# Optimization experiments

Hardware: AMD Instinct MI355X
Metric: run time of the kernel (lower is better)

Reference implementation:

```python
import jax, jax.numpy as jnp
from jax import lax
import numpy as np

WIN = 15
PAD = WIN // 2  # floor(15/2) = 7


def _box_sum(x):
    """Sum over a 15x15 window, stride 1, zero padding 7 (same as F.conv2d
    with an all-ones [1,1,15,15] filter). Done separably (H then W) for
    efficiency; math is identical to the dense ones-filter conv."""
    kh = jnp.ones((1, 1, WIN, 1), x.dtype)
    kw = jnp.ones((1, 1, 1, WIN), x.dtype)
    x = lax.conv_general_dilated(x, kh, (1, 1), [(PAD, PAD), (0, 0)])
    x = lax.conv_general_dilated(x, kw, (1, 1), [(0, 0), (PAD, PAD)])
    return x


def setup_inputs() -> dict:
    key = jax.random.key(0)
    k1, k2 = jax.random.split(key)
    B, C, H, W = 16, 1, 512, 512
    I = jax.random.uniform(k1, (B, C, H, W), dtype=jnp.float32)
    J = jax.random.uniform(k2, (B, C, H, W), dtype=jnp.float32)
    return {"I": I, "J": J}


def reference(I, J):
    win_size = jnp.asarray(WIN * WIN, I.dtype)

    I_sum = _box_sum(I)
    J_sum = _box_sum(J)
    I2_sum = _box_sum(I * I)
    J2_sum = _box_sum(J * J)
    IJ_sum = _box_sum(I * J)

    u_I = I_sum / win_size
    u_J = J_sum / win_size

    cross = IJ_sum - u_J * I_sum - u_I * J_sum + u_I * u_J * win_size
    I_var = I2_sum - 2 * u_I * I_sum + u_I * u_I * win_size
    J_var = J2_sum - 2 * u_J * J_sum + u_J * u_J * win_size

    # NOTE: faithful to the torch code — cc is a GLOBAL scalar ratio,
    # so torch.mean(cc) == cc.
    cc = jnp.sum(cross) / jnp.sqrt(jnp.sum(I_var) * jnp.sum(J_var))
    return -cc
```

## Files before the change

### kernel.cpp

```cpp
#include <hip/hip_runtime.h>
#include <math.h>


#define IMG_H 512
#define IMG_W 512
#define NB    16
#define TW    64
#define TH    32
#define HALO  7
#define SPAN_R 46
#define SPAN_C 78
#define LSTR  78
#define VSTR  79
#define NTX   8
#define NTY   16
#define NBLK  (NB * NTX * NTY)

__device__ __forceinline__ float winw(int i) {
    int a = i < 7 ? i : 7;
    int b = (511 - i) < 7 ? (511 - i) : 7;
    return (float)(a + b + 1);
}

__global__ __launch_bounds__(256) void ncc_main(const float* __restrict__ I,
                                                const float* __restrict__ J,
                                                float* __restrict__ partials) {
    __shared__ float lI[SPAN_R * LSTR];
    __shared__ float lJ[SPAN_R * LSTR];
    __shared__ float vI[TH * VSTR];
    __shared__ float vJ[TH * VSTR];
    __shared__ float red[4 * 6];

    const int tid = threadIdx.x;
    const int tx = blockIdx.x, ty = blockIdx.y, bz = blockIdx.z;
    const int R0 = ty * TH - HALO;
    const int C0 = tx * TW - HALO;
    const float* Ib = I + (size_t)bz * IMG_H * IMG_W;
    const float* Jb = J + (size_t)bz * IMG_H * IMG_W;

    float a0 = 0.f, a1 = 0.f, a2 = 0.f;

    for (int k = tid; k < SPAN_R * SPAN_C; k += 256) {
        int r = k / SPAN_C;
        int c = k - r * SPAN_C;
        int gr = R0 + r, gc = C0 + c;
        float iv = 0.0f, jv = 0.0f;
        if ((unsigned)gr < (unsigned)IMG_H && (unsigned)gc < (unsigned)IMG_W) {
            int gidx = gr * IMG_W + gc;
            iv = Ib[gidx];
            jv = Jb[gidx];
        }
        lI[r * LSTR + c] = iv;
        lJ[r * LSTR + c] = jv;
        if (r >= HALO && r < HALO + TH && c >= HALO && c < HALO + TW) {
            float w = winw(gr) * winw(gc);
            a0 += iv * jv * w;
            a1 += iv * iv * w;
            a2 += jv * jv * w;
        }
    }
    __syncthreads();

    {
        int cid = tid % SPAN_C;
        int chunk = tid / SPAN_C;
        if (chunk < 3) {
            int r0 = chunk * 11;
            int nr = (chunk == 2) ? 10 : 11;
            float sI = 0.0f, sJ = 0.0f;
            #pragma unroll
            for (int dr = 0; dr < 15; ++dr) {
                sI += lI[(r0 + dr) * LSTR + cid];
                sJ += lJ[(r0 + dr) * LSTR + cid];
            }
            vI[r0 * VSTR + cid] = sI;
            vJ[r0 * VSTR + cid] = sJ;
            for (int r = r0 + 1; r < r0 + nr; ++r) {
                sI += lI[(r + 14) * LSTR + cid] - lI[(r - 1) * LSTR + cid];
                sJ += lJ[(r + 14) * LSTR + cid] - lJ[(r - 1) * LSTR + cid];
                vI[r * VSTR + cid] = sI;
                vJ[r * VSTR + cid] = sJ;
            }
        }
    }
    __syncthreads();

    float a3 = 0.f, a4 = 0.f, a5 = 0.f;
    {
        int r = tid & 31;
        int ch = tid >> 5;
        int c0 = ch * 8;
        int base = r * VSTR + c0;
        float va[22], vb[22];
        #pragma unroll
        for (int i = 0; i < 22; ++i) {
            va[i] = vI[base + i];
            vb[i] = vJ[base + i];
        }
        float sI = 0.0f, sJ = 0.0f;
        #pragma unroll
        for (int i = 0; i < 15; ++i) { sI += va[i]; sJ += vb[i]; }
        a3 += sI * sJ;
        a4 += sI * sI;
        a5 += sJ * sJ;
        #pragma unroll
        for (int i = 1; i < 8; ++i) {
            sI += va[i + 14] - va[i - 1];
            sJ += vb[i + 14] - vb[i - 1];
            a3 += sI * sJ;
            a4 += sI * sI;
            a5 += sJ * sJ;
        }
    }

    float vals[6] = {a0, a1, a2, a3, a4, a5};
    #pragma unroll
    for (int k = 0; k < 6; ++k) {
        float v = vals[k];
        #pragma unroll
        for (int off = 32; off > 0; off >>= 1) v += __shfl_down(v, off, 64);
        vals[k] = v;
    }
    int wave = tid >> 6, lane = tid & 63;
    if (lane == 0) {
        #pragma unroll
        for (int k = 0; k < 6; ++k) red[wave * 6 + k] = vals[k];
    }
    __syncthreads();
    if (tid == 0) {
        int bidx = (bz * NTY + ty) * NTX + tx;
        #pragma unroll
        for (int k = 0; k < 6; ++k) {
            partials[bidx * 6 + k] = red[k] + red[6 + k] + red[12 + k] + red[18 + k];
        }
    }
}

__global__ __launch_bounds__(256) void ncc_finalize(const float* __restrict__ partials,
                                                    float* __restrict__ out) {
    __shared__ double red[4 * 6];
    int tid = threadIdx.x;
    double acc[6] = {0, 0, 0, 0, 0, 0};
    for (int b = tid; b < NBLK; b += 256) {
        #pragma unroll
        for (int k = 0; k < 6; ++k) acc[k] += (double)partials[b * 6 + k];
    }
    #pragma unroll
    for (int k = 0; k < 6; ++k) {
        double v = acc[k];
        #pragma unroll
        for (int off = 32; off > 0; off >>= 1) v += __shfl_down(v, off, 64);
        acc[k] = v;
    }
    int wave = tid >> 6, lane = tid & 63;
    if (lane == 0) {
        #pragma unroll
        for (int k = 0; k < 6; ++k) red[wave * 6 + k] = acc[k];
    }
    __syncthreads();
    if (tid == 0) {
        double s[6];
        #pragma unroll
        for (int k = 0; k < 6; ++k) s[k] = red[k] + red[6 + k] + red[12 + k] + red[18 + k];
        double A = s[0], Bv = s[1], Cv = s[2], D = s[3], E = s[4], F = s[5];
        double num = A - D / 225.0;
        double varI = Bv - E / 225.0;
        double varJ = Cv - F / 225.0;
        double cc = num / sqrt(varI * varJ);
        out[0] = (float)(-cc);
    }
}

extern "C" void kernel_launch(void* const* d_in, const int* in_sizes, int n_in,
                              void* d_out, int out_size, void* d_ws, size_t ws_size,
                              hipStream_t stream) {
    const float* I = (const float*)d_in[0];
    const float* J = (const float*)d_in[1];
    float* partials = (float*)d_ws;

    dim3 grid(NTX, NTY, NB);
    ncc_main<<<grid, 256, 0, stream>>>(I, J, partials);
    ncc_finalize<<<1, 256, 0, stream>>>(partials, (float*)d_out);
}
```

Baseline: 99.64 us.

## Compute horizontal box sums in registers via float4 loads and fuse finalize via atomic counter

Each thread now loads a 32-wide row segment of I and J with float4 reads into registers and computes the horizontal 15-wide running sums directly. It writes interleaved float2 partial sums to shared memory, replacing the old full-tile staging and the vertical-first shared-memory pass. The separate finalize kernel is removed: the last block, found with an atomic counter and thread fences, does the double-precision global reduction. This cuts shared-memory traffic and one kernel launch, but adds a memset, atomic serialization, and heavy register use (64 floats per thread) that may lower occupancy.

```diff
diff --git a/kernel.cpp b/kernel.cpp
--- a/kernel.cpp
+++ b/kernel.cpp
@@ -7,11 +7,8 @@
 #define NB    16
 #define TW    64
 #define TH    32
-#define HALO  7
 #define SPAN_R 46
-#define SPAN_C 78
-#define LSTR  78
-#define VSTR  79
+#define STR2  65
 #define NTX   8
 #define NTY   16
 #define NBLK  (NB * NTX * NTY)
@@ -24,92 +21,87 @@
 
 __global__ __launch_bounds__(256) void ncc_main(const float* __restrict__ I,
                                                 const float* __restrict__ J,
-                                                float* __restrict__ partials) {
-    __shared__ float lI[SPAN_R * LSTR];
-    __shared__ float lJ[SPAN_R * LSTR];
-    __shared__ float vI[TH * VSTR];
-    __shared__ float vJ[TH * VSTR];
-    __shared__ float red[4 * 6];
+                                                float* __restrict__ partials,
+                                                unsigned* __restrict__ counter,
+                                                float* __restrict__ out) {
+    __shared__ float2 H[SPAN_R * STR2];
+    __shared__ float redf[4 * 6];
+    __shared__ double redd[4 * 6];
+    __shared__ int lastflag;
 
     const int tid = threadIdx.x;
     const int tx = blockIdx.x, ty = blockIdx.y, bz = blockIdx.z;
-    const int R0 = ty * TH - HALO;
-    const int C0 = tx * TW - HALO;
+    const int R0 = ty * TH - 7;
+    const int C0 = tx * TW;
     const float* Ib = I + (size_t)bz * IMG_H * IMG_W;
     const float* Jb = J + (size_t)bz * IMG_H * IMG_W;
 
     float a0 = 0.f, a1 = 0.f, a2 = 0.f;
 
-    for (int k = tid; k < SPAN_R * SPAN_C; k += 256) {
-        int r = k / SPAN_C;
-        int c = k - r * SPAN_C;
-        int gr = R0 + r, gc = C0 + c;
-        float iv = 0.0f, jv = 0.0f;
-        if ((unsigned)gr < (unsigned)IMG_H && (unsigned)gc < (unsigned)IMG_W) {
-            int gidx = gr * IMG_W + gc;
-            iv = Ib[gidx];
-            jv = Jb[gidx];
+    if (tid < SPAN_R * 4) {
+        int r = tid >> 2;
+        int run = tid & 3;
+        int gr = R0 + r;
+        int c0 = C0 + run * 16;
+        int gb = c0 - 8;
+        bool rowok = ((unsigned)gr < (unsigned)IMG_H);
+        float rI[32], rJ[32];
+        #pragma unroll
+        for (int q = 0; q < 8; ++q) {
+            int gc = gb + q * 4;
+            float4 iv = make_float4(0.f, 0.f, 0.f, 0.f);
+            float4 jv = make_float4(0.f, 0.f, 0.f, 0.f);
+            if (rowok && (unsigned)gc < (unsigned)IMG_W) {
+                iv = *reinterpret_cast<const float4*>(Ib + gr * IMG_W + gc);
+                jv = *reinterpret_cast<const float4*>(Jb + gr * IMG_W + gc);
+            }
+            rI[4 * q + 0] = iv.x; rI[4 * q + 1] = iv.y;
+            rI[4 * q + 2] = iv.z; rI[4 * q + 3] = iv.w;
+            rJ[4 * q + 0] = jv.x; rJ[4 * q + 1] = jv.y;
+            rJ[4 * q + 2] = jv.z; rJ[4 * q + 3] = jv.w;
         }
-        lI[r * LSTR + c] = iv;
-        lJ[r * LSTR + c] = jv;
-        if (r >= HALO && r < HALO + TH && c >= HALO && c < HALO + TW) {
-            float w = winw(gr) * winw(gc);
-            a0 += iv * jv * w;
-            a1 += iv * iv * w;
-            a2 += jv * jv * w;
+        if (r >= 7 && r < 7 + TH) {
+            float wr = winw(gr);
+            #pragma unroll
+            for (int t = 0; t < 16; ++t) {
+                float w = wr * winw(c0 + t);
+                float iv = rI[t + 8], jv = rJ[t + 8];
+                a0 += iv * jv * w;
+                a1 += iv * iv * w;
+                a2 += jv * jv * w;
+            }
         }
-    }
-    __syncthreads();
-
-    {
-        int cid = tid % SPAN_C;
-        int chunk = tid / SPAN_C;
-        if (chunk < 3) {
-            int r0 = chunk * 11;
-            int nr = (chunk == 2) ? 10 : 11;
-            float sI = 0.0f, sJ = 0.0f;
-            #pragma unroll
-            for (int dr = 0; dr < 15; ++dr) {
-                sI += lI[(r0 + dr) * LSTR + cid];
-                sJ += lJ[(r0 + dr) * LSTR + cid];
-            }
-            vI[r0 * VSTR + cid] = sI;
-            vJ[r0 * VSTR + cid] = sJ;
-            for (int r = r0 + 1; r < r0 + nr; ++r) {
-                sI += lI[(r + 14) * LSTR + cid] - lI[(r - 1) * LSTR + cid];
-                sJ += lJ[(r + 14) * LSTR + cid] - lJ[(r - 1) * LSTR + cid];
-                vI[r * VSTR + cid] = sI;
-                vJ[r * VSTR + cid] = sJ;
-            }
+        float hI = 0.f, hJ = 0.f;
+        #pragma unroll
+        for (int d = 1; d <= 15; ++d) { hI += rI[d]; hJ += rJ[d]; }
+        float2* Hrow = &H[r * STR2 + run * 16];
+        Hrow[0] = make_float2(hI, hJ);
+        #pragma unroll
+        for (int t = 1; t < 16; ++t) {
+            hI += rI[t + 15] - rI[t];
+            hJ += rJ[t + 15] - rJ[t];
+            Hrow[t] = make_float2(hI, hJ);
         }
     }
     __syncthreads();
 
     float a3 = 0.f, a4 = 0.f, a5 = 0.f;
     {
-        int r = tid & 31;
-        int ch = tid >> 5;
-        int c0 = ch * 8;
-        int base = r * VSTR + c0;
-        float va[22], vb[22];
+        int c = tid & 63;
+        int band = tid >> 6;
+        int rb = band * 8;
+        float2 win[22];
         #pragma unroll
-        for (int i = 0; i < 22; ++i) {
-            va[i] = vI[base + i];
-            vb[i] = vJ[base + i];
-        }
-        float sI = 0.0f, sJ = 0.0f;
+        for (int i = 0; i < 22; ++i) win[i] = H[(rb + i) * STR2 + c];
+        float sI = 0.f, sJ = 0.f;
         #pragma unroll
-        for (int i = 0; i < 15; ++i) { sI += va[i]; sJ += vb[i]; }
-        a3 += sI * sJ;
-        a4 += sI * sI;
-        a5 += sJ * sJ;
+        for (int i = 0; i < 15; ++i) { sI += win[i].x; sJ += win[i].y; }
+        a3 += sI * sJ; a4 += sI * sI; a5 += sJ * sJ;
         #pragma unroll
         for (int i = 1; i < 8; ++i) {
-            sI += va[i + 14] - va[i - 1];
-            sJ += vb[i + 14] - vb[i - 1];
-            a3 += sI * sJ;
-            a4 += sI * sI;
-            a5 += sJ * sJ;
+            sI += win[i + 14].x - win[i - 1].x;
+            sJ += win[i + 14].y - win[i - 1].y;
+            a3 += sI * sJ; a4 += sI * sI; a5 += sJ * sJ;
         }
     }
 
@@ -124,50 +116,52 @@
     int wave = tid >> 6, lane = tid & 63;
     if (lane == 0) {
         #pragma unroll
-        for (int k = 0; k < 6; ++k) red[wave * 6 + k] = vals[k];
+        for (int k = 0; k < 6; ++k) redf[wave * 6 + k] = vals[k];
     }
     __syncthreads();
     if (tid == 0) {
         int bidx = (bz * NTY + ty) * NTX + tx;
         #pragma unroll
         for (int k = 0; k < 6; ++k) {
-            partials[bidx * 6 + k] = red[k] + red[6 + k] + red[12 + k] + red[18 + k];
+            partials[bidx * 6 + k] = redf[k] + redf[6 + k] + redf[12 + k] + redf[18 + k];
         }
-    }
-}
-
-__global__ __launch_bounds__(256) void ncc_finalize(const float* __restrict__ partials,
-                                                    float* __restrict__ out) {
-    __shared__ double red[4 * 6];
-    int tid = threadIdx.x;
-    double acc[6] = {0, 0, 0, 0, 0, 0};
-    for (int b = tid; b < NBLK; b += 256) {
-        #pragma unroll
-        for (int k = 0; k < 6; ++k) acc[k] += (double)partials[b * 6 + k];
-    }
-    #pragma unroll
-    for (int k = 0; k < 6; ++k) {
-        double v = acc[k];
-        #pragma unroll
-        for (int off = 32; off > 0; off >>= 1) v += __shfl_down(v, off, 64);
-        acc[k] = v;
-    }
-    int wave = tid >> 6, lane = tid & 63;
-    if (lane == 0) {
-        #pragma unroll
-        for (int k = 0; k < 6; ++k) red[wave * 6 + k] = acc[k];
+        __threadfence();
+        unsigned old = atomicAdd(counter, 1u);
+        lastflag = (old == (unsigned)(NBLK - 1)) ? 1 : 0;
     }
     __syncthreads();
-    if (tid == 0) {
-        double s[6];
+
+    if (lastflag) {
+        __threadfence();
+        double acc[6] = {0, 0, 0, 0, 0, 0};
+        for (int b = tid; b < NBLK; b += 256) {
+            #pragma unroll
+            for (int k = 0; k < 6; ++k) acc[k] += (double)partials[b * 6 + k];
+        }
         #pragma unroll
-        for (int k = 0; k < 6; ++k) s[k] = red[k] + red[6 + k] + red[12 + k] + red[18 + k];
-        double A = s[0], Bv = s[1], Cv = s[2], D = s[3], E = s[4], F = s[5];
-        double num = A - D / 225.0;
-        double varI = Bv - E / 225.0;
-        double varJ = Cv - F / 225.0;
-        double cc = num / sqrt(varI * varJ);
-        out[0] = (float)(-cc);
+        for (int k = 0; k < 6; ++k) {
+            double v = acc[k];
+            #pragma unroll
+            for (int off = 32; off > 0; off >>= 1) v += __shfl_down(v, off, 64);
+            acc[k] = v;
+        }
+        if (lane == 0) {
+            #pragma unroll
+            for (int k = 0; k < 6; ++k) redd[wave * 6 + k] = acc[k];
+        }
+        __syncthreads();
+        if (tid == 0) {
+            double s[6];
+            #pragma unroll
+            for (int k = 0; k < 6; ++k)
+                s[k] = redd[k] + redd[6 + k] + redd[12 + k] + redd[18 + k];
+            double A = s[0], Bv = s[1], Cv = s[2], D = s[3], E = s[4], F = s[5];
+            double num = A - D / 225.0;
+            double varI = Bv - E / 225.0;
+            double varJ = Cv - F / 225.0;
+            double cc = num / sqrt(varI * varJ);
+            out[0] = (float)(-cc);
+        }
     }
 }
 
@@ -177,8 +171,9 @@
     const float* I = (const float*)d_in[0];
     const float* J = (const float*)d_in[1];
     float* partials = (float*)d_ws;
+    unsigned* counter = (unsigned*)((char*)d_ws + NBLK * 6 * sizeof(float));
 
+    hipMemsetAsync(counter, 0, sizeof(unsigned), stream);
     dim3 grid(NTX, NTY, NB);
-    ncc_main<<<grid, 256, 0, stream>>>(I, J, partials);
-    ncc_finalize<<<1, 256, 0, stream>>>(partials, (float*)d_out);
+    ncc_main<<<grid, 256, 0, stream>>>(I, J, partials, counter, (float*)d_out);
 }
```

Result: slower. 136.0 us (+36.5%).

## Split box-filter NCC into separate vertical and horizontal pass kernels

Applied to the files above, without the earlier changes.

Replaces the single fused tiled kernel, which loads a haloed 2D tile into LDS, with two kernels. A vertical running-sum kernel streams columns and writes float2 column sums to a global workspace. A horizontal kernel then reads those back to finish the row sums. This removes the redundant halo loads, about 75% extra from the 46x78 tile per 32x64 output, but adds a full round trip through global memory: 32 MB written and then read back. It also adds one more kernel launch.

```diff
diff --git a/kernel.cpp b/kernel.cpp
--- a/kernel.cpp
+++ b/kernel.cpp
@@ -5,16 +5,13 @@
 #define IMG_H 512
 #define IMG_W 512
 #define NB    16
-#define TW    64
-#define TH    32
-#define HALO  7
-#define SPAN_R 46
-#define SPAN_C 78
-#define LSTR  78
-#define VSTR  79
-#define NTX   8
-#define NTY   16
-#define NBLK  (NB * NTX * NTY)
+#define BAND  16
+#define NBANDS (IMG_H / BAND)
+#define NVBLK (NB * NBANDS * 2)
+#define HTW   64
+#define HTH   32
+#define HSTR  81
+#define NHBLK (NB * (IMG_H / HTH) * (IMG_W / HTW))
 
 __device__ __forceinline__ float winw(int i) {
     int a = i < 7 ? i : 7;
@@ -22,100 +19,125 @@
     return (float)(a + b + 1);
 }
 
-__global__ __launch_bounds__(256) void ncc_main(const float* __restrict__ I,
+__global__ __launch_bounds__(256) void ncc_vert(const float* __restrict__ I,
                                                 const float* __restrict__ J,
-                                                float* __restrict__ partials) {
-    __shared__ float lI[SPAN_R * LSTR];
-    __shared__ float lJ[SPAN_R * LSTR];
-    __shared__ float vI[TH * VSTR];
-    __shared__ float vJ[TH * VSTR];
-    __shared__ float red[4 * 6];
-
+                                                float2* __restrict__ V,
+                                                float* __restrict__ P1) {
+    __shared__ float redf[4 * 3];
     const int tid = threadIdx.x;
-    const int tx = blockIdx.x, ty = blockIdx.y, bz = blockIdx.z;
-    const int R0 = ty * TH - HALO;
-    const int C0 = tx * TW - HALO;
+    const int c = blockIdx.x * 256 + tid;
+    const int O0 = blockIdx.y * BAND;
+    const int bz = blockIdx.z;
     const float* Ib = I + (size_t)bz * IMG_H * IMG_W;
     const float* Jb = J + (size_t)bz * IMG_H * IMG_W;
-
+    float2* Vb = V + (size_t)bz * IMG_H * IMG_W;
+
+    const float wc = winw(c);
+    float sI = 0.f, sJ = 0.f;
     float a0 = 0.f, a1 = 0.f, a2 = 0.f;
 
-    for (int k = tid; k < SPAN_R * SPAN_C; k += 256) {
-        int r = k / SPAN_C;
-        int c = k - r * SPAN_C;
-        int gr = R0 + r, gc = C0 + c;
-        float iv = 0.0f, jv = 0.0f;
-        if ((unsigned)gr < (unsigned)IMG_H && (unsigned)gc < (unsigned)IMG_W) {
-            int gidx = gr * IMG_W + gc;
-            iv = Ib[gidx];
-            jv = Jb[gidx];
-        }
-        lI[r * LSTR + c] = iv;
-        lJ[r * LSTR + c] = jv;
-        if (r >= HALO && r < HALO + TH && c >= HALO && c < HALO + TW) {
-            float w = winw(gr) * winw(gc);
+    int rstart = O0 - 8; if (rstart < 0) rstart = 0;
+    for (int r = rstart; r < O0 + 7; ++r) {
+        float iv = Ib[r * IMG_W + c];
+        float jv = Jb[r * IMG_W + c];
+        sI += iv; sJ += jv;
+        if (O0 == 0) {
+            float w = winw(r) * wc;
             a0 += iv * jv * w;
             a1 += iv * iv * w;
             a2 += jv * jv * w;
         }
     }
-    __syncthreads();
-
-    {
-        int cid = tid % SPAN_C;
-        int chunk = tid / SPAN_C;
-        if (chunk < 3) {
-            int r0 = chunk * 11;
-            int nr = (chunk == 2) ? 10 : 11;
-            float sI = 0.0f, sJ = 0.0f;
-            #pragma unroll
-            for (int dr = 0; dr < 15; ++dr) {
-                sI += lI[(r0 + dr) * LSTR + cid];
-                sJ += lJ[(r0 + dr) * LSTR + cid];
-            }
-            vI[r0 * VSTR + cid] = sI;
-            vJ[r0 * VSTR + cid] = sJ;
-            for (int r = r0 + 1; r < r0 + nr; ++r) {
-                sI += lI[(r + 14) * LSTR + cid] - lI[(r - 1) * LSTR + cid];
-                sJ += lJ[(r + 14) * LSTR + cid] - lJ[(r - 1) * LSTR + cid];
-                vI[r * VSTR + cid] = sI;
-                vJ[r * VSTR + cid] = sJ;
-            }
-        }
-    }
-    __syncthreads();
-
-    float a3 = 0.f, a4 = 0.f, a5 = 0.f;
+
+    #pragma unroll 4
+    for (int o = O0; o < O0 + BAND; ++o) {
+        int rT = o + 7, rB = o - 8;
+        float ivT = 0.f, jvT = 0.f;
+        if (rT < IMG_H) {
+            ivT = Ib[rT * IMG_W + c];
+            jvT = Jb[rT * IMG_W + c];
+            float w = winw(rT) * wc;
+            a0 += ivT * jvT * w;
+            a1 += ivT * ivT * w;
+            a2 += jvT * jvT * w;
+        }
+        float ivB = 0.f, jvB = 0.f;
+        if (rB >= 0) {
+            ivB = Ib[rB * IMG_W + c];
+            jvB = Jb[rB * IMG_W + c];
+        }
+        sI += ivT - ivB;
+        sJ += jvT - jvB;
+        Vb[o * IMG_W + c] = make_float2(sI, sJ);
+    }
+
+    float vals[3] = {a0, a1, a2};
+    #pragma unroll
+    for (int k = 0; k < 3; ++k) {
+        float v = vals[k];
+        #pragma unroll
+        for (int off = 32; off > 0; off >>= 1) v += __shfl_down(v, off, 64);
+        vals[k] = v;
+    }
+    int wave = tid >> 6, lane = tid & 63;
+    if (lane == 0) {
+        #pragma unroll
+        for (int k = 0; k < 3; ++k) redf[wave * 3 + k] = vals[k];
+    }
+    __syncthreads();
+    if (tid == 0) {
+        int bid = (bz * NBANDS + blockIdx.y) * 2 + blockIdx.x;
+        #pragma unroll
+        for (int k = 0; k < 3; ++k)
+            P1[bid * 3 + k] = redf[k] + redf[3 + k] + redf[6 + k] + redf[9 + k];
+    }
+}
+
+__global__ __launch_bounds__(256) void ncc_horiz(const float2* __restrict__ V,
+                                                 float* __restrict__ P2) {
+    __shared__ float2 buf[HTH * HSTR];
+    __shared__ float redf[4 * 3];
+    const int tid = threadIdx.x;
+    const int tx = blockIdx.x, ty = blockIdx.y, bz = blockIdx.z;
+    const int C0 = tx * HTW - 8;
+    const int Rt = ty * HTH;
+    const float2* Vb = V + (size_t)bz * IMG_H * IMG_W;
+
+    for (int k = tid; k < HTH * 40; k += 256) {
+        int r = k / 40, f = k - (k / 40) * 40;
+        int vc = C0 + 2 * f;
+        float4 x = make_float4(0.f, 0.f, 0.f, 0.f);
+        if ((unsigned)vc < (unsigned)(IMG_W - 1)) {
+            x = *reinterpret_cast<const float4*>(&Vb[(Rt + r) * IMG_W + vc]);
+        }
+        buf[r * HSTR + 2 * f]     = make_float2(x.x, x.y);
+        buf[r * HSTR + 2 * f + 1] = make_float2(x.z, x.w);
+    }
+    __syncthreads();
+
+    float d0 = 0.f, e0 = 0.f, f0 = 0.f;
     {
         int r = tid & 31;
         int ch = tid >> 5;
-        int c0 = ch * 8;
-        int base = r * VSTR + c0;
-        float va[22], vb[22];
-        #pragma unroll
-        for (int i = 0; i < 22; ++i) {
-            va[i] = vI[base + i];
-            vb[i] = vJ[base + i];
-        }
-        float sI = 0.0f, sJ = 0.0f;
-        #pragma unroll
-        for (int i = 0; i < 15; ++i) { sI += va[i]; sJ += vb[i]; }
-        a3 += sI * sJ;
-        a4 += sI * sI;
-        a5 += sJ * sJ;
+        int base = r * HSTR + ch * 8 + 1;
+        float2 v[22];
+        #pragma unroll
+        for (int i = 0; i < 22; ++i) v[i] = buf[base + i];
+        float sI = 0.f, sJ = 0.f;
+        #pragma unroll
+        for (int i = 0; i < 15; ++i) { sI += v[i].x; sJ += v[i].y; }
+        d0 += sI * sJ; e0 += sI * sI; f0 += sJ * sJ;
         #pragma unroll
         for (int i = 1; i < 8; ++i) {
-            sI += va[i + 14] - va[i - 1];
-            sJ += vb[i + 14] - vb[i - 1];
-            a3 += sI * sJ;
-            a4 += sI * sI;
-            a5 += sJ * sJ;
-        }
-    }
-
-    float vals[6] = {a0, a1, a2, a3, a4, a5};
+            sI += v[i + 14].x - v[i - 1].x;
+            sJ += v[i + 14].y - v[i - 1].y;
+            d0 += sI * sJ; e0 += sI * sI; f0 += sJ * sJ;
+        }
+    }
+
+    float vals[3] = {d0, e0, f0};
     #pragma unroll
-    for (int k = 0; k < 6; ++k) {
+    for (int k = 0; k < 3; ++k) {
         float v = vals[k];
         #pragma unroll
         for (int off = 32; off > 0; off >>= 1) v += __shfl_down(v, off, 64);
@@ -124,26 +146,30 @@
     int wave = tid >> 6, lane = tid & 63;
     if (lane == 0) {
         #pragma unroll
-        for (int k = 0; k < 6; ++k) red[wave * 6 + k] = vals[k];
+        for (int k = 0; k < 3; ++k) redf[wave * 3 + k] = vals[k];
     }
     __syncthreads();
     if (tid == 0) {
-        int bidx = (bz * NTY + ty) * NTX + tx;
-        #pragma unroll
-        for (int k = 0; k < 6; ++k) {
-            partials[bidx * 6 + k] = red[k] + red[6 + k] + red[12 + k] + red[18 + k];
-        }
-    }
-}
-
-__global__ __launch_bounds__(256) void ncc_finalize(const float* __restrict__ partials,
+        int bid = ((bz * (IMG_H / HTH)) + ty) * (IMG_W / HTW) + tx;
+        #pragma unroll
+        for (int k = 0; k < 3; ++k)
+            P2[bid * 3 + k] = redf[k] + redf[3 + k] + redf[6 + k] + redf[9 + k];
+    }
+}
+
+__global__ __launch_bounds__(256) void ncc_finalize(const float* __restrict__ P1,
+                                                    const float* __restrict__ P2,
                                                     float* __restrict__ out) {
     __shared__ double red[4 * 6];
     int tid = threadIdx.x;
     double acc[6] = {0, 0, 0, 0, 0, 0};
-    for (int b = tid; b < NBLK; b += 256) {
-        #pragma unroll
-        for (int k = 0; k < 6; ++k) acc[k] += (double)partials[b * 6 + k];
+    for (int b = tid; b < NVBLK; b += 256) {
+        #pragma unroll
+        for (int k = 0; k < 3; ++k) acc[k] += (double)P1[b * 3 + k];
+    }
+    for (int b = tid; b < NHBLK; b += 256) {
+        #pragma unroll
+        for (int k = 0; k < 3; ++k) acc[3 + k] += (double)P2[b * 3 + k];
     }
     #pragma unroll
     for (int k = 0; k < 6; ++k) {
@@ -176,9 +202,13 @@
                               hipStream_t stream) {
     const float* I = (const float*)d_in[0];
     const float* J = (const float*)d_in[1];
-    float* partials = (float*)d_ws;
-
-    dim3 grid(NTX, NTY, NB);
-    ncc_main<<<grid, 256, 0, stream>>>(I, J, partials);
-    ncc_finalize<<<1, 256, 0, stream>>>(partials, (float*)d_out);
-}
+    float2* V = (float2*)d_ws;
+    float* P1 = (float*)((char*)d_ws + (size_t)NB * IMG_H * IMG_W * sizeof(float2));
+    float* P2 = P1 + NVBLK * 3;
+
+    dim3 gv(2, NBANDS, NB);
+    ncc_vert<<<gv, 256, 0, stream>>>(I, J, V, P1);
+    dim3 gh(IMG_W / HTW, IMG_H / HTH, NB);
+    ncc_horiz<<<gh, 256, 0, stream>>>(V, P2);
+    ncc_finalize<<<1, 256, 0, stream>>>(P1, P2, (float*)d_out);
+}
```

Result: slower. 105.6 us (+6.0%).

## Compute vertical box sums directly from global loads into registers, dropping raw smem tile

Applied to the files above, without the earlier changes.

Each of 234 threads now loads a column strip of 25 rows straight from global memory into registers and computes the vertical 15-row running sums there, skipping the raw input staging in shared memory and one barrier. The vertical sums are stored as interleaved float2 in a smaller shared buffer, and launch bounds request 4 blocks per SM to raise occupancy. The trade-off is more register pressure, since every 78-column band reloads 14 overlapping halo rows from global/L2, and 22 threads per block sit idle in the load phase.

```diff
diff --git a/kernel.cpp b/kernel.cpp
--- a/kernel.cpp
+++ b/kernel.cpp
@@ -7,11 +7,8 @@
 #define NB    16
 #define TW    64
 #define TH    32
-#define HALO  7
-#define SPAN_R 46
 #define SPAN_C 78
-#define LSTR  78
-#define VSTR  79
+#define S2    79
 #define NTX   8
 #define NTY   16
 #define NBLK  (NB * NTX * NTY)
@@ -22,64 +19,66 @@
     return (float)(a + b + 1);
 }
 
-__global__ __launch_bounds__(256) void ncc_main(const float* __restrict__ I,
-                                                const float* __restrict__ J,
-                                                float* __restrict__ partials) {
-    __shared__ float lI[SPAN_R * LSTR];
-    __shared__ float lJ[SPAN_R * LSTR];
-    __shared__ float vI[TH * VSTR];
-    __shared__ float vJ[TH * VSTR];
-    __shared__ float red[4 * 6];
+__global__ __launch_bounds__(256, 4) void ncc_main(const float* __restrict__ I,
+                                                   const float* __restrict__ J,
+                                                   float* __restrict__ partials) {
+    __shared__ float2 V[TH * S2];
+    __shared__ float redf[4 * 6];
 
     const int tid = threadIdx.x;
     const int tx = blockIdx.x, ty = blockIdx.y, bz = blockIdx.z;
-    const int R0 = ty * TH - HALO;
-    const int C0 = tx * TW - HALO;
+    const int R0 = ty * TH;
+    const int C0 = tx * TW;
     const float* Ib = I + (size_t)bz * IMG_H * IMG_W;
     const float* Jb = J + (size_t)bz * IMG_H * IMG_W;
 
     float a0 = 0.f, a1 = 0.f, a2 = 0.f;
 
-    for (int k = tid; k < SPAN_R * SPAN_C; k += 256) {
-        int r = k / SPAN_C;
-        int c = k - r * SPAN_C;
-        int gr = R0 + r, gc = C0 + c;
-        float iv = 0.0f, jv = 0.0f;
-        if ((unsigned)gr < (unsigned)IMG_H && (unsigned)gc < (unsigned)IMG_W) {
-            int gidx = gr * IMG_W + gc;
-            iv = Ib[gidx];
-            jv = Jb[gidx];
-        }
-        lI[r * LSTR + c] = iv;
-        lJ[r * LSTR + c] = jv;
-        if (r >= HALO && r < HALO + TH && c >= HALO && c < HALO + TW) {
-            float w = winw(gr) * winw(gc);
-            a0 += iv * jv * w;
-            a1 += iv * iv * w;
-            a2 += jv * jv * w;
-        }
-    }
-    __syncthreads();
+    {
+        int band = tid / SPAN_C;
+        int cl = tid - band * SPAN_C;
+        if (band < 3) {
+            const int r0     = (band == 0) ? 0 : (band == 1) ? 11 : 22;
+            const int nr     = (band == 2) ? 10 : 11;
+            const int nraw   = nr + 14;
+            const int own_lo = (band == 0) ? 0 : (band == 1) ? 18 : 29;
+            const int own_hi = (band == 0) ? 17 : (band == 1) ? 28 : 31;
+            const int gc = C0 - 7 + cl;
+            const bool colok = (unsigned)gc < (unsigned)IMG_W;
+            const bool own_c = (cl >= 7 && cl <= 70);
+            const float wc = colok ? winw(gc) : 0.f;
+            const float* Ip = Ib + gc;
+            const float* Jp = Jb + gc;
 
-    {
-        int cid = tid % SPAN_C;
-        int chunk = tid / SPAN_C;
-        if (chunk < 3) {
-            int r0 = chunk * 11;
-            int nr = (chunk == 2) ? 10 : 11;
-            float sI = 0.0f, sJ = 0.0f;
+            float rI[25], rJ[25];
             #pragma unroll
-            for (int dr = 0; dr < 15; ++dr) {
-                sI += lI[(r0 + dr) * LSTR + cid];
-                sJ += lJ[(r0 + dr) * LSTR + cid];
+            for (int t = 0; t < 25; ++t) {
+                int rel = r0 - 7 + t;
+                int gr = R0 + rel;
+                float iv = 0.f, jv = 0.f;
+                if (t < nraw && colok && (unsigned)gr < (unsigned)IMG_H) {
+                    iv = Ip[gr * IMG_W];
+                    jv = Jp[gr * IMG_W];
+                }
+                rI[t] = iv; rJ[t] = jv;
+                if (t < nraw && own_c && rel >= own_lo && rel <= own_hi) {
+                    float w = winw(gr) * wc;
+                    a0 += iv * jv * w;
+                    a1 += iv * iv * w;
+                    a2 += jv * jv * w;
+                }
             }
-            vI[r0 * VSTR + cid] = sI;
-            vJ[r0 * VSTR + cid] = sJ;
-            for (int r = r0 + 1; r < r0 + nr; ++r) {
-                sI += lI[(r + 14) * LSTR + cid] - lI[(r - 1) * LSTR + cid];
-                sJ += lJ[(r + 14) * LSTR + cid] - lJ[(r - 1) * LSTR + cid];
-                vI[r * VSTR + cid] = sI;
-                vJ[r * VSTR + cid] = sJ;
+            float sI = 0.f, sJ = 0.f;
+            #pragma unroll
+            for (int t = 0; t < 15; ++t) { sI += rI[t]; sJ += rJ[t]; }
+            V[r0 * S2 + cl] = make_float2(sI, sJ);
+            #pragma unroll
+            for (int k = 1; k < 11; ++k) {
+                if (k < nr) {
+                    sI += rI[14 + k] - rI[k - 1];
+                    sJ += rJ[14 + k] - rJ[k - 1];
+                    V[(r0 + k) * S2 + cl] = make_float2(sI, sJ);
+                }
             }
         }
     }
@@ -89,27 +88,19 @@
     {
         int r = tid & 31;
         int ch = tid >> 5;
-        int c0 = ch * 8;
-        int base = r * VSTR + c0;
-        float va[22], vb[22];
+        int base = r * S2 + ch * 8;
+        float2 v[22];
         #pragma unroll
-        for (int i = 0; i < 22; ++i) {
-            va[i] = vI[base + i];
-            vb[i] = vJ[base + i];
-        }
-        float sI = 0.0f, sJ = 0.0f;
+        for (int i = 0; i < 22; ++i) v[i] = V[base + i];
+        float sI = 0.f, sJ = 0.f;
         #pragma unroll
-        for (int i = 0; i < 15; ++i) { sI += va[i]; sJ += vb[i]; }
-        a3 += sI * sJ;
-        a4 += sI * sI;
-        a5 += sJ * sJ;
+        for (int i = 0; i < 15; ++i) { sI += v[i].x; sJ += v[i].y; }
+        a3 += sI * sJ; a4 += sI * sI; a5 += sJ * sJ;
         #pragma unroll
         for (int i = 1; i < 8; ++i) {
-            sI += va[i + 14] - va[i - 1];
-            sJ += vb[i + 14] - vb[i - 1];
-            a3 += sI * sJ;
-            a4 += sI * sI;
-            a5 += sJ * sJ;
+            sI += v[i + 14].x - v[i - 1].x;
+            sJ += v[i + 14].y - v[i - 1].y;
+            a3 += sI * sJ; a4 += sI * sI; a5 += sJ * sJ;
         }
     }
 
@@ -124,14 +115,14 @@
     int wave = tid >> 6, lane = tid & 63;
     if (lane == 0) {
         #pragma unroll
-        for (int k = 0; k < 6; ++k) red[wave * 6 + k] = vals[k];
+        for (int k = 0; k < 6; ++k) redf[wave * 6 + k] = vals[k];
     }
     __syncthreads();
     if (tid == 0) {
         int bidx = (bz * NTY + ty) * NTX + tx;
         #pragma unroll
         for (int k = 0; k < 6; ++k) {
-            partials[bidx * 6 + k] = red[k] + red[6 + k] + red[12 + k] + red[18 + k];
+            partials[bidx * 6 + k] = redf[k] + redf[6 + k] + redf[12 + k] + redf[18 + k];
         }
     }
 }
```

After: 93.35 us. 6.3% less time.
